# Kernel tuning notes

Measured on AMD Instinct MI355X. Metric: run time of the kernel, lower is better.

Reference implementation:

```python
import jax, jax.numpy as jnp
import numpy as np

L, D, H, DH, W, G, FF = 2, 768, 12, 64, 256, 64, 3072  # W = one-sided window (attention_window=512)
B, S = 2, 4096
NEG = -1e9


def setup_inputs() -> dict:
    key = jax.random.key(0)
    ks = jax.random.split(key, 16)
    inp = {}
    inp['hidden_states'] = jax.random.normal(ks[0], (B, S, D), jnp.float32)
    # HF Longformer convention: <0 masked, >0 global, 0 local. First G tokens are global.
    inp['attention_mask'] = jnp.zeros((B, S), jnp.float32).at[:, :G].set(1.0)
    inp['padding_len'] = 0
    inp['level_hierarchy'] = 0
    def w(k, shape):
        return (jax.random.normal(k, shape, jnp.float32) * 0.02)
    for i, n in enumerate(['Wq', 'Wk', 'Wv', 'Wqg', 'Wkg', 'Wvg', 'Wo']):
        inp[n] = w(ks[1 + i], (L, D, D))
        inp['b' + n[1:].lower()] = jnp.zeros((L, D), jnp.float32)
    inp['Wi'] = w(ks[8], (L, D, FF)); inp['bi'] = jnp.zeros((L, FF), jnp.float32)
    inp['Wo2'] = w(ks[9], (L, FF, D)); inp['bo2'] = jnp.zeros((L, D), jnp.float32)
    for n in ['ln1', 'ln2']:
        inp[n + '_g'] = jnp.ones((L, D), jnp.float32)
        inp[n + '_b'] = jnp.zeros((L, D), jnp.float32)
    return inp


def _ln(x, g, b):
    mu = jnp.mean(x, -1, keepdims=True)
    var = jnp.mean(jnp.square(x - mu), -1, keepdims=True)
    return (x - mu) * jax.lax.rsqrt(var + 1e-5) * g + b


def _chunk3(x, nc, w):
    # x: [..., S, d] -> [..., nc, 3w, d]: keys of chunks (c-1, c, c+1), zero-padded at the ends
    shp = x.shape
    xr = x.reshape(shp[:-2] + (nc, w, shp[-1]))
    pad = [(0, 0)] * xr.ndim
    pad[-3] = (1, 1)
    xp = jnp.pad(xr, pad)
    return jnp.concatenate([xp[..., :-2, :, :], xp[..., 1:-1, :, :], xp[..., 2:, :, :]], axis=-2)


def _layer(h, mask, Wq, bq, Wk, bk, Wv, bv, Wqg, bqg, Wkg, bkg, Wvg, bvg,
           Wo, bo, ln1_g, ln1_b, Wi, bi, Wo2, bo2, ln2_g, ln2_b):
    Bb, Ss, Dd = h.shape
    nc = Ss // W
    scale = 1.0 / np.sqrt(DH)
    def heads(x):
        return x.reshape(Bb, Ss, H, DH).transpose(0, 2, 1, 3)  # [B,H,S,dh]
    q = heads(h @ Wq + bq) * scale
    k = heads(h @ Wk + bk)
    v = heads(h @ Wv + bv)
    # --- sliding-window (banded) attention, chunked ---
    qc = q.reshape(Bb, H, nc, W, DH)
    k3 = _chunk3(k, nc, W)  # [B,H,nc,3W,dh]
    v3 = _chunk3(v, nc, W)
    local = jnp.einsum('bhcid,bhcjd->bhcij', qc, k3)  # [B,H,nc,W,3W]
    i = jnp.arange(W)[:, None]
    j = jnp.arange(3 * W)[None, :]
    band_ok = jnp.abs(j - W - i) <= W                              # [W,3W]
    keypos = jnp.arange(nc)[:, None, None] * W + (j - W)[None]     # [nc,1,3W]
    in_range = (keypos >= 0) & (keypos < Ss)
    # masked and global keys are removed from the windowed attention (handled via global cols)
    key_local = _chunk3((mask == 0).astype(h.dtype)[..., None], nc, W)[..., 0] > 0.5  # [B,nc,3W]
    valid = band_ok[None, None] & in_range[None] & key_local[:, :, None, :]  # [B,nc,W,3W]
    local = jnp.where(valid[:, None], local, NEG)
    # --- global key columns (every token attends to the G global tokens) ---
    kg, vg = k[:, :, :G], v[:, :, :G]
    sg = jnp.einsum('bhsd,bhgd->bhsg', q, kg).reshape(Bb, H, nc, W, G)
    probs = jax.nn.softmax(jnp.concatenate([sg, local], axis=-1), axis=-1)
    pg, pl = probs[..., :G], probs[..., G:]
    out = (jnp.einsum('bhcig,bhgd->bhcid', pg, vg)
           + jnp.einsum('bhcij,bhcjd->bhcid', pl, v3)).reshape(Bb, H, Ss, DH)
    # --- global token rows: full attention with dedicated global projections ---
    qg = heads(h @ Wqg + bqg)[:, :, :G] * scale
    kgf = heads(h @ Wkg + bkg)
    vgf = heads(h @ Wvg + bvg)
    add = jnp.where(mask < 0, NEG, 0.0)[:, None, None, :]
    pgl = jax.nn.softmax(jnp.einsum('bhgd,bhsd->bhgs', qg, kgf) + add, axis=-1)
    out = out.at[:, :, :G].set(jnp.einsum('bhgs,bhsd->bhgd', pgl, vgf))
    out = jnp.where((mask < 0)[:, None, :, None], 0.0, out)
    attn = out.transpose(0, 2, 1, 3).reshape(Bb, Ss, Dd) @ Wo + bo
    h = _ln(attn + h, ln1_g, ln1_b)
    ff = jax.nn.gelu(h @ Wi + bi, approximate=False) @ Wo2 + bo2
    return _ln(ff + h, ln2_g, ln2_b)


def reference(hidden_states, attention_mask, padding_len, level_hierarchy,
              Wq, bq, Wk, bk, Wv, bv, Wqg, bqg, Wkg, bkg, Wvg, bvg,
              Wo, bo, ln1_g, ln1_b, Wi, bi, Wo2, bo2, ln2_g, ln2_b):
    h = hidden_states
    for l in range(L):
        h = _layer(h, attention_mask,
                   Wq[l], bq[l], Wk[l], bk[l], Wv[l], bv[l],
                   Wqg[l], bqg[l], Wkg[l], bkg[l], Wvg[l], bvg[l],
                   Wo[l], bo[l], ln1_g[l], ln1_b[l],
                   Wi[l], bi[l], Wo2[l], bo2[l], ln2_g[l], ln2_b[l])
    if padding_len > 0:
        h = h[:, :-padding_len]
    return h
```

## Files before the change

### kernel.cpp

```cpp
#include <hip/hip_runtime.h>

#define B_ 2
#define S_ 4096
#define D_ 768
#define H_ 12
#define DH_ 64
#define W_ 256
#define G_ 64
#define FF_ 3072
#define L_ 2
#define M_ (B_*S_)
#define NEGV -1e9f
#define NSPLIT 16

typedef short bf16x8 __attribute__((ext_vector_type(8)));
typedef float f32x4 __attribute__((ext_vector_type(4)));
typedef unsigned short u16;
typedef unsigned short u16x4 __attribute__((ext_vector_type(4)));

__device__ __forceinline__ u16 f2bf(float f) {
  union { float f; unsigned u; } a; a.f = f;
  unsigned r = a.u + 0x7FFFu + ((a.u >> 16) & 1u);
  return (u16)(r >> 16);
}
__device__ __forceinline__ float b2f(u16 u) {
  union { unsigned u; float f; } a; a.u = ((unsigned)u) << 16;
  return a.f;
}

__device__ __forceinline__ f32x4 mfma16(bf16x8 a, bf16x8 b, f32x4 c) {
  return __builtin_amdgcn_mfma_f32_16x16x32_bf16(a, b, c, 0, 0, 0);
}

__device__ __forceinline__ void gload16(const u16* g, u16* l) {
  __builtin_amdgcn_global_load_lds((const __attribute__((address_space(1))) void*)g,
                                   (__attribute__((address_space(3))) void*)l, 16, 0, 0);
}

__device__ __forceinline__ int xcd_swz(int bid, int nwg) {
  if ((nwg & 7) == 0) {
    int cpx = nwg >> 3;
    bid = (bid & 7) * cpx + (bid >> 3);
  }
  return bid;
}

struct Ptr7 { const float* p[7]; };
__global__ __launch_bounds__(256) void wtrans7(Ptr7 in, u16* __restrict__ out) {
  __shared__ float tile[32][33];
  int z = blockIdx.z;
  int slab = z >> 1, l = z & 1;
  const float* src = in.p[slab] + (size_t)l * D_ * D_;
  u16* dst = out + (size_t)z * D_ * D_;
  int k0 = blockIdx.y * 32, n0 = blockIdx.x * 32;
  int tx = threadIdx.x, ty = threadIdx.y;
#pragma unroll
  for (int i = 0; i < 4; i++)
    tile[ty + i*8][tx] = src[(size_t)(k0 + ty + i*8) * D_ + n0 + tx];
  __syncthreads();
#pragma unroll
  for (int i = 0; i < 4; i++)
    dst[(size_t)(n0 + ty + i*8) * D_ + k0 + tx] = f2bf(tile[tx][ty + i*8]);
}

__global__ __launch_bounds__(256) void wtrans(const float* __restrict__ in,
                                              u16* __restrict__ out, int K, int N) {
  __shared__ float tile[32][33];
  size_t base = (size_t)blockIdx.z * K * N;
  int k0 = blockIdx.y * 32, n0 = blockIdx.x * 32;
  int tx = threadIdx.x, ty = threadIdx.y;
#pragma unroll
  for (int i = 0; i < 4; i++)
    tile[ty + i*8][tx] = in[base + (size_t)(k0 + ty + i*8) * N + n0 + tx];
  __syncthreads();
#pragma unroll
  for (int i = 0; i < 4; i++)
    out[base + (size_t)(n0 + ty + i*8) * K + k0 + tx] = f2bf(tile[tx][ty + i*8]);
}

__global__ __launch_bounds__(256) void conv_b(const float* __restrict__ in,
                                              u16* __restrict__ outb, int n4) {
  int i = blockIdx.x * 256 + threadIdx.x;
  if (i >= n4) return;
  float4 v = ((const float4*)in)[i];
  u16x4 o;
  o[0] = f2bf(v.x); o[1] = f2bf(v.y); o[2] = f2bf(v.z); o[3] = f2bf(v.w);
  ((u16x4*)outb)[i] = o;
}

template <int MODE>
__device__ __forceinline__ float epi_post(float v) {
  if (MODE == 2) return v * 0.125f;
  if (MODE == 3) {
    float y = 0.79788456f * (v + 0.044715f * v * v * v);
    float e = __expf(fminf(2.f * y, 20.f));
    return v * e / (e + 1.f);
  }
  return v;
}

struct Bias6 { const float* p[6]; };

template <int MODE, int NW>
__global__ __launch_bounds__(512, 4) void gemm_wide(const u16* __restrict__ A,
                                                    const u16* __restrict__ Wbase,
                                                    Bias6 bp,
                                                    u16* __restrict__ OutBase,
                                                    int Kdim, int Nstride, int l) {
  __shared__ u16 sh[36864];
  int gx = gridDim.x;
  int bid = blockIdx.x + blockIdx.y * gx;
  bid = xcd_swz(bid, gx * gridDim.y);
  int bxx = bid % gx, by = bid / gx;
  int bm = by * 128;
  int widx, bn;
  const u16* Bt; u16* Cb; const float* bias;
  bool qscale = false;
  if (NW == 5) {
    widx = bxx / 3;
    bn = (bxx % 3) * 256;
    int slab;
    if (widx == 5) {
      if (by != 0 && by != 32) return;
      slab = 3; qscale = true;
    } else {
      slab = widx + (widx >= 3 ? 1 : 0);
      qscale = (widx == 0);
    }
    Bt = Wbase + ((size_t)slab * L_ + l) * (size_t)D_ * D_;
    Cb = OutBase + (size_t)slab * M_ * D_;
    bias = bp.p[widx];
  } else {
    widx = 0;
    bn = bxx * 256;
    Bt = Wbase; Cb = OutBase; bias = bp.p[0];
  }
  int tid = threadIdx.x;
  int lane = tid & 63, wid = tid >> 6;
  int wr = wid >> 2, wc = wid & 3;
  int lr = lane & 15, lg = lane >> 4;

  int fA = tid;
  int lA_ = fA >> 3, uA = (fA & 7) ^ (lA_ & 7);
  int rowA = lA_ * 2 + (uA >> 2), c8A = uA & 3;
  const u16* srcA = A + (size_t)(bm + rowA) * Kdim + c8A * 8;
  int fB0 = tid, fB1 = tid + 512;
  int lB0 = fB0 >> 3, uB0 = (fB0 & 7) ^ (lB0 & 7);
  int rB0 = lB0 * 2 + (uB0 >> 2), c8B0 = uB0 & 3;
  int lB1 = fB1 >> 3, uB1 = (fB1 & 7) ^ (lB1 & 7);
  int rB1 = lB1 * 2 + (uB1 >> 2), c8B1 = uB1 & 3;
  const u16* srcB0 = Bt + (size_t)(bn + rB0) * Kdim + c8B0 * 8;
  const u16* srcB1 = Bt + (size_t)(bn + rB1) * Kdim + c8B1 * 8;

  auto stage = [&](int kt, int buf) {
    int k1 = kt << 5;
    gload16(srcA + k1, &sh[buf * 4096 + fA * 8]);
    gload16(srcB0 + k1, &sh[12288 + buf * 8192 + fB0 * 8]);
    gload16(srcB1 + k1, &sh[12288 + buf * 8192 + fB1 * 8]);
  };

  int offa[4], offb[4];
#pragma unroll
  for (int i = 0; i < 4; i++) {
    int ra = wr * 64 + i * 16 + lr;
    int la = ra >> 1, sa = (((ra & 1) << 2) | lg) ^ (la & 7);
    offa[i] = la * 64 + sa * 8;
    int rb = wc * 64 + i * 16 + lr;
    int lb = rb >> 1, sb = (((rb & 1) << 2) | lg) ^ (lb & 7);
    offb[i] = lb * 64 + sb * 8;
  }

  int nt = Kdim >> 5;
  f32x4 acc[4][4] = {};

  stage(0, 0);
  if (nt > 1) stage(1, 1);

  for (int t = 0; t < nt; t++) {
    int cb = t % 3;
    if (t + 2 < nt) {
      stage(t + 2, (t + 2) % 3);
      asm volatile("s_waitcnt vmcnt(6)" ::: "memory");
    } else if (t + 1 < nt) {
      asm volatile("s_waitcnt vmcnt(3)" ::: "memory");
    } else {
      asm volatile("s_waitcnt vmcnt(0)" ::: "memory");
    }
    __builtin_amdgcn_s_barrier();
    __builtin_amdgcn_sched_barrier(0);
    const u16* ab = sh + cb * 4096;
    const u16* bb = sh + 12288 + cb * 8192;
    bf16x8 a[4], b[4];
#pragma unroll
    for (int i = 0; i < 4; i++) a[i] = *(const bf16x8*)&ab[offa[i]];
#pragma unroll
    for (int j = 0; j < 4; j++) b[j] = *(const bf16x8*)&bb[offb[j]];
    __builtin_amdgcn_s_setprio(1);
#pragma unroll
    for (int i = 0; i < 4; i++)
#pragma unroll
      for (int j = 0; j < 4; j++)
        acc[i][j] = mfma16(a[i], b[j], acc[i][j]);
    __builtin_amdgcn_s_setprio(0);
    __builtin_amdgcn_sched_barrier(0);
    __builtin_amdgcn_s_barrier();
    __builtin_amdgcn_sched_barrier(0);
  }

  int r0 = bm + wr * 64, c0 = bn + wc * 64;
  int cr = (lane >> 4) * 4, cc = lane & 15;
  float sc = qscale ? 0.125f : 1.0f;
#pragma unroll
  for (int j = 0; j < 4; j++) {
    int col = c0 + j * 16 + cc;
    float bv = bias[col];
#pragma unroll
    for (int i = 0; i < 4; i++)
#pragma unroll
      for (int r = 0; r < 4; r++) {
        size_t off = (size_t)(r0 + i * 16 + cr + r) * Nstride + col;
        Cb[off] = f2bf(epi_post<MODE>((acc[i][j][r] + bv) * sc));
      }
  }
}

template <int MODE>
__global__ __launch_bounds__(256) void gemm_pipe(const u16* __restrict__ A,
                                                 const u16* __restrict__ Bt,
                                                 const float* __restrict__ bias,
                                                 u16* __restrict__ Cb,
                                                 int Ndim, int Kdim, int rowTileStride) {
  __shared__ u16 sh[24576];
  int gx = gridDim.x;
  int bid = blockIdx.x + blockIdx.y * gx;
  bid = xcd_swz(bid, gx * gridDim.y);
  int bm = (bid / gx) * rowTileStride * 128;
  int bn = (bid % gx) * 128;
  int tid = threadIdx.x;
  int lane = tid & 63, w = tid >> 6;
  int r0w = (w >> 1) * 64, c0w = (w & 1) * 64;
  int lr = lane & 15, lg = lane >> 4;

  int f0 = tid, l0 = f0 >> 3, s0 = (f0 & 7) ^ (l0 & 7);
  int row0 = (l0 << 1) | (s0 >> 2), c0s = (s0 & 3) * 8;
  int f1 = tid + 256, l1 = f1 >> 3, s1 = (f1 & 7) ^ (l1 & 7);
  int row1 = (l1 << 1) | (s1 >> 2), c1s = (s1 & 3) * 8;
  const u16* A0 = A + (size_t)(bm + row0) * Kdim + c0s;
  const u16* A1 = A + (size_t)(bm + row1) * Kdim + c1s;
  const u16* B0 = Bt + (size_t)(bn + row0) * Kdim + c0s;
  const u16* B1 = Bt + (size_t)(bn + row1) * Kdim + c1s;

  int offa[4], offb[4];
#pragma unroll
  for (int i = 0; i < 4; i++) {
    int ra = r0w + i * 16 + lr;
    int la = ra >> 1, sa = ((ra & 1) << 2) | lg;
    offa[i] = la * 64 + (sa ^ (la & 7)) * 8;
    int rb = c0w + i * 16 + lr;
    int lb = rb >> 1, sb = ((rb & 1) << 2) | lg;
    offb[i] = lb * 64 + (sb ^ (lb & 7)) * 8;
  }

  auto stage = [&](int kt, int buf) {
    int k1 = kt << 5;
    u16* ab = sh + buf * 4096;
    u16* bb = sh + 12288 + buf * 4096;
    gload16(A0 + k1, &ab[tid * 8]);
    gload16(A1 + k1, &ab[tid * 8 + 2048]);
    gload16(B0 + k1, &bb[tid * 8]);
    gload16(B1 + k1, &bb[tid * 8 + 2048]);
  };

  int nt = Kdim >> 5;
  f32x4 acc[4][4] = {};

  stage(0, 0);
  if (nt > 1) stage(1, 1);

  for (int t = 0; t < nt; t++) {
    int cb = t % 3;
    if (t + 2 < nt) {
      stage(t + 2, (t + 2) % 3);
      asm volatile("s_waitcnt vmcnt(8)" ::: "memory");
    } else if (t + 1 < nt) {
      asm volatile("s_waitcnt vmcnt(4)" ::: "memory");
    } else {
      asm volatile("s_waitcnt vmcnt(0)" ::: "memory");
    }
    __builtin_amdgcn_s_barrier();
    __builtin_amdgcn_sched_barrier(0);
    const u16* ab = sh + cb * 4096;
    const u16* bb = sh + 12288 + cb * 4096;
    bf16x8 a[4], b[4];
#pragma unroll
    for (int i = 0; i < 4; i++) a[i] = *(const bf16x8*)&ab[offa[i]];
#pragma unroll
    for (int j = 0; j < 4; j++) b[j] = *(const bf16x8*)&bb[offb[j]];
#pragma unroll
    for (int i = 0; i < 4; i++)
#pragma unroll
      for (int j = 0; j < 4; j++)
        acc[i][j] = mfma16(a[i], b[j], acc[i][j]);
    __builtin_amdgcn_sched_barrier(0);
    __builtin_amdgcn_s_barrier();
    __builtin_amdgcn_sched_barrier(0);
  }

  int cr = (lane >> 4) * 4, cc = lane & 15;
#pragma unroll
  for (int j = 0; j < 4; j++) {
    int col = c0w + j * 16 + cc;
    float bv = bias[bn + col];
#pragma unroll
    for (int i = 0; i < 4; i++)
#pragma unroll
      for (int r = 0; r < 4; r++) {
        int row = r0w + i * 16 + cr + r;
        int chunk = (col >> 3) ^ (row & 15);
        sh[row * 128 + chunk * 8 + (col & 7)] =
            f2bf(epi_post<MODE>(acc[i][j][r] + bv));
      }
  }
  __syncthreads();
  {
    int row = tid >> 1, half = tid & 1;
    u16* gro = Cb + (size_t)(bm + row) * Ndim + bn + half * 64;
#pragma unroll
    for (int c = 0; c < 8; c++) {
      int lc = half * 8 + c;
      int pc = lc ^ (row & 15);
      bf16x8 v = *(const bf16x8*)&sh[row * 128 + pc * 8];
      *(bf16x8*)(gro + c * 8) = v;
    }
  }
}

__global__ __launch_bounds__(128) void attn_local(const u16* __restrict__ qb,
                                                  const u16* __restrict__ kb_,
                                                  const u16* __restrict__ vb,
                                                  const float* __restrict__ mask,
                                                  u16* __restrict__ ao) {
  int bid = blockIdx.x + blockIdx.y * gridDim.x;
  bid = xcd_swz(bid, 1536);
  int cx = bid & 63, bh = bid >> 6;
  int c = cx >> 2, sub = cx & 3;
  int b = bh / H_, h = bh % H_;
  int tid = threadIdx.x;
  int w = tid >> 6, lane = tid & 63;
  int lr = lane & 15, lg = lane >> 4;

  __shared__ u16 vtT[64][72];
  __shared__ u16 plds[2][32][72];
  __shared__ unsigned char vflag[576];

  int base_off = sub * 64;
  int kwin0 = c * W_ - W_;
  for (int i = tid; i < 576; i += 128) {
    int kp = kwin0 + base_off + i;
    vflag[i] = (kp >= 0 && kp < S_ && mask[b * S_ + kp] == 0.0f) ? 1 : 0;
  }

  size_t hoff = (size_t)b * S_ * D_ + h * DH_;
  int qrow0 = c * W_ + base_off + w * 32;
  bf16x8 aq[2][2];
#pragma unroll
  for (int fi = 0; fi < 2; fi++)
#pragma unroll
    for (int ks = 0; ks < 2; ks++)
      aq[fi][ks] = *(const bf16x8*)(qb + hoff + (size_t)(qrow0 + fi * 16 + lr) * D_ + ks * 32 + lg * 8);

  int K0 = kwin0 + base_off;
  int kb_lo = (K0 < 0) ? (1 + ((-K0) >> 6)) : 1;
  int kb_hi = 9;
  { int hi = 1 + ((S_ - 64 - K0) >> 6); if (hi < 9) kb_hi = hi; }
  int niter = 1 + (kb_hi - kb_lo + 1);

  int stg_k4 = tid >> 3, stg_j = tid & 7;
  int stg_dh0 = stg_j * 8;

  float ls[2][4];
  f32x4 o[2][4] = {};
#pragma unroll
  for (int fi = 0; fi < 2; fi++)
#pragma unroll
    for (int r = 0; r < 4; r++) ls[fi][r] = 0.f;

  bf16x8 ck0[4], ck1[4], nk0[4], nk1[4], cv[4], nv[4];
#pragma unroll
  for (int nj = 0; nj < 4; nj++) {
    const u16* ks8 = kb_ + hoff + (size_t)(nj * 16 + lr) * D_ + lg * 8;
    ck0[nj] = *(const bf16x8*)(ks8);
    ck1[nj] = *(const bf16x8*)(ks8 + 32);
  }
#pragma unroll
  for (int p = 0; p < 4; p++)
    cv[p] = *(const bf16x8*)(vb + hoff + (size_t)(p * 16 + stg_k4) * D_ + stg_dh0);

  for (int it = 0; it < niter; it++) {
    int kb = (it == 0) ? 0 : (kb_lo + it - 1);

    __builtin_amdgcn_s_barrier();
#pragma unroll
    for (int p = 0; p < 4; p++) {
      int key = p * 16 + stg_k4;
      u16* basep = &vtT[stg_dh0][key ^ (stg_j << 3)];
#pragma unroll
      for (int e = 0; e < 8; e++) basep[e * 72] = (u16)cv[p][e];
    }
    if (it + 1 < niter) {
      int kb2 = kb_lo + it;
      int ks2 = K0 + (kb2 - 1) * 64;
#pragma unroll
      for (int nj = 0; nj < 4; nj++) {
        const u16* ks8 = kb_ + hoff + (size_t)(ks2 + nj * 16 + lr) * D_ + lg * 8;
        nk0[nj] = *(const bf16x8*)(ks8);
        nk1[nj] = *(const bf16x8*)(ks8 + 32);
      }
#pragma unroll
      for (int p = 0; p < 4; p++)
        nv[p] = *(const bf16x8*)(vb + hoff + (size_t)(ks2 + p * 16 + stg_k4) * D_ + stg_dh0);
    }
    asm volatile("s_waitcnt lgkmcnt(0)" ::: "memory");
    __builtin_amdgcn_s_barrier();
    __builtin_amdgcn_sched_barrier(0);

    f32x4 sc[2][4];
#pragma unroll
    for (int fi = 0; fi < 2; fi++)
#pragma unroll
      for (int nj = 0; nj < 4; nj++) {
        f32x4 t = {};
        t = mfma16(aq[fi][0], ck0[nj], t);
        t = mfma16(aq[fi][1], ck1[nj], t);
        sc[fi][nj] = t;
      }

    if (kb >= 2 && kb <= 8) {
#pragma unroll
      for (int nj = 0; nj < 4; nj++) {
        bool kv = vflag[(kb - 1) * 64 + nj * 16 + lr] != 0;
#pragma unroll
        for (int fi = 0; fi < 2; fi++)
#pragma unroll
          for (int r = 0; r < 4; r++)
            sc[fi][nj][r] = kv ? sc[fi][nj][r] : NEGV;
      }
    } else if (kb > 0) {
#pragma unroll
      for (int nj = 0; nj < 4; nj++) {
        int fidx = (kb - 1) * 64 + nj * 16 + lr;
        int koff = base_off + fidx;
        bool kv = vflag[fidx] != 0;
#pragma unroll
        for (int fi = 0; fi < 2; fi++)
#pragma unroll
          for (int r = 0; r < 4; r++) {
            int wq = base_off + w * 32 + fi * 16 + lg * 4 + r;
            if (!(kv && koff >= wq && koff <= wq + 2 * W_)) sc[fi][nj][r] = NEGV;
          }
      }
    }

#pragma unroll
    for (int fi = 0; fi < 2; fi++)
#pragma unroll
      for (int r = 0; r < 4; r++) {
        float ps = 0.f;
#pragma unroll
        for (int nj = 0; nj < 4; nj++) {
          float p = __expf(sc[fi][nj][r]);
          sc[fi][nj][r] = p;
          ps += p;
        }
#pragma unroll
        for (int d = 1; d < 16; d <<= 1) ps += __shfl_xor(ps, d);
        ls[fi][r] += ps;
      }

#pragma unroll
    for (int fi = 0; fi < 2; fi++)
#pragma unroll
      for (int nj = 0; nj < 4; nj++)
#pragma unroll
        for (int r = 0; r < 4; r++)
          plds[w][fi * 16 + lg * 4 + r][nj * 16 + lr] = f2bf(sc[fi][nj][r]);
    asm volatile("s_waitcnt lgkmcnt(0)" ::: "memory");
    __builtin_amdgcn_sched_barrier(0);

    bf16x8 ap[2][2];
#pragma unroll
    for (int fi = 0; fi < 2; fi++)
#pragma unroll
      for (int ks = 0; ks < 2; ks++)
        ap[fi][ks] = *(const bf16x8*)&plds[w][fi * 16 + lr][ks * 32 + lg * 8];
#pragma unroll
    for (int dj = 0; dj < 4; dj++) {
      int xr = ((dj * 16 + lr) >> 3) & 7;
#pragma unroll
      for (int ks = 0; ks < 2; ks++) {
        bf16x8 bv = *(const bf16x8*)&vtT[dj * 16 + lr][(ks * 32 + lg * 8) ^ (xr << 3)];
        o[0][dj] = mfma16(ap[0][ks], bv, o[0][dj]);
        o[1][dj] = mfma16(ap[1][ks], bv, o[1][dj]);
      }
    }

    if (it + 1 < niter) {
#pragma unroll
      for (int j = 0; j < 4; j++) {
        ck0[j] = nk0[j]; ck1[j] = nk1[j]; cv[j] = nv[j];
      }
    }
  }

#pragma unroll
  for (int fi = 0; fi < 2; fi++)
#pragma unroll
    for (int dj = 0; dj < 4; dj++)
#pragma unroll
      for (int r = 0; r < 4; r++) {
        int row = qrow0 + fi * 16 + lg * 4 + r;
        float v = o[fi][dj][r] / ls[fi][r];
        ao[hoff + (size_t)row * D_ + dj * 16 + lr] = f2bf(v);
      }
}

__global__ __launch_bounds__(128) void attn_gsplit(const u16* __restrict__ qg,
                                                   const u16* __restrict__ kg,
                                                   const u16* __restrict__ vg,
                                                   float* __restrict__ opart,
                                                   float* __restrict__ lpart) {
  int sp = blockIdx.x, bh = blockIdx.y;
  int b = bh / H_, h = bh % H_;
  int tid = threadIdx.x, w = tid >> 6, lane = tid & 63;
  int lr = lane & 15, lg = lane >> 4;
  __shared__ u16 vtT[64][72];
  __shared__ u16 plds[2][32][72];
  size_t hoff = (size_t)b * S_ * D_ + h * DH_;
  int qrow0 = w * 32;
  bf16x8 aq[2][2];
#pragma unroll
  for (int fi = 0; fi < 2; fi++)
#pragma unroll
    for (int ks = 0; ks < 2; ks++)
      aq[fi][ks] = *(const bf16x8*)(qg + hoff + (size_t)(qrow0 + fi * 16 + lr) * D_ + ks * 32 + lg * 8);
  float ls[2][4];
  f32x4 o[2][4] = {};
#pragma unroll
  for (int fi = 0; fi < 2; fi++)
#pragma unroll
    for (int r = 0; r < 4; r++) ls[fi][r] = 0.f;

  int stg_k4 = tid >> 3, stg_j = tid & 7;
  int stg_dh0 = stg_j * 8;

  for (int kb = 0; kb < 4; kb++) {
    int kstart = sp * 256 + kb * 64;
    __syncthreads();
#pragma unroll
    for (int p = 0; p < 4; p++) {
      int key = p * 16 + stg_k4;
      bf16x8 row = *(const bf16x8*)(vg + hoff + (size_t)(kstart + key) * D_ + stg_dh0);
      u16* basep = &vtT[stg_dh0][key ^ (stg_j << 3)];
#pragma unroll
      for (int e = 0; e < 8; e++) basep[e * 72] = (u16)row[e];
    }
    __syncthreads();

    bf16x8 bk0[4], bk1[4];
#pragma unroll
    for (int nj = 0; nj < 4; nj++) {
      const u16* ks8 = kg + hoff + (size_t)(kstart + nj * 16 + lr) * D_ + lg * 8;
      bk0[nj] = *(const bf16x8*)(ks8);
      bk1[nj] = *(const bf16x8*)(ks8 + 32);
    }
    f32x4 sc[2][4];
#pragma unroll
    for (int fi = 0; fi < 2; fi++)
#pragma unroll
      for (int nj = 0; nj < 4; nj++) {
        f32x4 t = {};
        t = mfma16(aq[fi][0], bk0[nj], t);
        t = mfma16(aq[fi][1], bk1[nj], t);
        sc[fi][nj] = t;
      }
#pragma unroll
    for (int fi = 0; fi < 2; fi++)
#pragma unroll
      for (int r = 0; r < 4; r++) {
        float ps = 0.f;
#pragma unroll
        for (int nj = 0; nj < 4; nj++) {
          float p = __expf(sc[fi][nj][r]);
          sc[fi][nj][r] = p;
          ps += p;
        }
#pragma unroll
        for (int d = 1; d < 16; d <<= 1) ps += __shfl_xor(ps, d);
        ls[fi][r] += ps;
      }
#pragma unroll
    for (int fi = 0; fi < 2; fi++)
#pragma unroll
      for (int nj = 0; nj < 4; nj++)
#pragma unroll
        for (int r = 0; r < 4; r++)
          plds[w][fi * 16 + lg * 4 + r][nj * 16 + lr] = f2bf(sc[fi][nj][r]);
    asm volatile("s_waitcnt lgkmcnt(0)" ::: "memory");
    __builtin_amdgcn_sched_barrier(0);
    bf16x8 ap[2][2];
#pragma unroll
    for (int fi = 0; fi < 2; fi++)
#pragma unroll
      for (int ks = 0; ks < 2; ks++)
        ap[fi][ks] = *(const bf16x8*)&plds[w][fi * 16 + lr][ks * 32 + lg * 8];
#pragma unroll
    for (int dj = 0; dj < 4; dj++) {
      int xr = ((dj * 16 + lr) >> 3) & 7;
#pragma unroll
      for (int ks = 0; ks < 2; ks++) {
        bf16x8 bv = *(const bf16x8*)&vtT[dj * 16 + lr][(ks * 32 + lg * 8) ^ (xr << 3)];
        o[0][dj] = mfma16(ap[0][ks], bv, o[0][dj]);
        o[1][dj] = mfma16(ap[1][ks], bv, o[1][dj]);
      }
    }
  }

  size_t pbase = (size_t)(bh * NSPLIT + sp) * 64;
#pragma unroll
  for (int fi = 0; fi < 2; fi++)
#pragma unroll
    for (int r = 0; r < 4; r++) {
      int row = qrow0 + fi * 16 + lg * 4 + r;
      if (lr == 0) lpart[pbase + row] = ls[fi][r];
#pragma unroll
      for (int dj = 0; dj < 4; dj++)
        opart[(pbase + row) * 64 + dj * 16 + lr] = o[fi][dj][r];
    }
}

__global__ __launch_bounds__(256) void attn_gcombine(const float* __restrict__ opart,
                                                     const float* __restrict__ lpart,
                                                     u16* __restrict__ ao) {
  int bh = blockIdx.x;
  int b = bh / H_, h = bh % H_;
  int t = threadIdx.x;
  __shared__ float lt[64];
  if (t < 64) {
    float lsum = 0.f;
#pragma unroll
    for (int sp = 0; sp < NSPLIT; sp++)
      lsum += lpart[(size_t)(bh * NSPLIT + sp) * 64 + t];
    lt[t] = lsum;
  }
  __syncthreads();
  int row = t >> 2, c0 = (t & 3) * 16;
  float acc[16] = {};
  for (int sp = 0; sp < NSPLIT; sp++) {
    const float* op = opart + ((size_t)(bh * NSPLIT + sp) * 64 + row) * 64 + c0;
#pragma unroll
    for (int j = 0; j < 16; j++) acc[j] += op[j];
  }
  float inv = 1.f / lt[row];
  size_t hoff = (size_t)b * S_ * D_ + h * DH_;
#pragma unroll
  for (int j = 0; j < 16; j++)
    ao[hoff + (size_t)row * D_ + c0 + j] = f2bf(acc[j] * inv);
}

__global__ __launch_bounds__(192) void ln_b(const u16* __restrict__ x,
                                            const u16* __restrict__ res,
                                            const float* __restrict__ gg,
                                            const float* __restrict__ bb,
                                            u16* __restrict__ outb,
                                            float* __restrict__ outf) {
  int row = blockIdx.x, t = threadIdx.x;
  const u16* xr = x + (size_t)row * D_;
  const u16* rr = res + (size_t)row * D_;
  u16x4 xv = *(const u16x4*)&xr[t * 4];
  u16x4 rv = *(const u16x4*)&rr[t * 4];
  float v[4];
#pragma unroll
  for (int e = 0; e < 4; e++) v[e] = b2f(xv[e]) + b2f(rv[e]);
  __shared__ float sha[3], shb[3];
  float s = v[0] + v[1] + v[2] + v[3];
#pragma unroll
  for (int d = 1; d < 64; d <<= 1) s += __shfl_xor(s, d);
  if ((t & 63) == 0) sha[t >> 6] = s;
  __syncthreads();
  float mu = (sha[0] + sha[1] + sha[2]) * (1.f / 768.f);
  float dd[4], s2 = 0.f;
#pragma unroll
  for (int e = 0; e < 4; e++) { dd[e] = v[e] - mu; s2 += dd[e] * dd[e]; }
#pragma unroll
  for (int d = 1; d < 64; d <<= 1) s2 += __shfl_xor(s2, d);
  if ((t & 63) == 0) shb[t >> 6] = s2;
  __syncthreads();
  float var = (shb[0] + shb[1] + shb[2]) * (1.f / 768.f);
  float rs = rsqrtf(var + 1e-5f);
  float4 gv = *(const float4*)&gg[t * 4];
  float4 bv = *(const float4*)&bb[t * 4];
  float y0 = dd[0] * rs * gv.x + bv.x;
  float y1 = dd[1] * rs * gv.y + bv.y;
  float y2 = dd[2] * rs * gv.z + bv.z;
  float y3 = dd[3] * rs * gv.w + bv.w;
  u16x4 ov;
  ov[0] = f2bf(y0); ov[1] = f2bf(y1); ov[2] = f2bf(y2); ov[3] = f2bf(y3);
  *(u16x4*)&outb[(size_t)row * D_ + t * 4] = ov;
  if (outf) {
    float4 of = {y0, y1, y2, y3};
    *(float4*)&outf[(size_t)row * D_ + t * 4] = of;
  }
}

extern "C" void kernel_launch(void* const* d_in, const int* in_sizes, int n_in,
                              void* d_out, int out_size, void* d_ws, size_t ws_size,
                              hipStream_t stream) {
  (void)in_sizes; (void)n_in; (void)out_size; (void)ws_size;
  const float* hidden = (const float*)d_in[0];
  const float* mask   = (const float*)d_in[1];
  const float* Wq  = (const float*)d_in[4];   const float* bq  = (const float*)d_in[5];
  const float* Wk  = (const float*)d_in[6];   const float* bk  = (const float*)d_in[7];
  const float* Wv  = (const float*)d_in[8];   const float* bv  = (const float*)d_in[9];
  const float* Wqg = (const float*)d_in[10];  const float* bqg = (const float*)d_in[11];
  const float* Wkg = (const float*)d_in[12];  const float* bkg = (const float*)d_in[13];
  const float* Wvg = (const float*)d_in[14];  const float* bvg = (const float*)d_in[15];
  const float* Wo  = (const float*)d_in[16];  const float* bo  = (const float*)d_in[17];
  const float* Wi  = (const float*)d_in[18];  const float* bi  = (const float*)d_in[19];
  const float* Wo2 = (const float*)d_in[20];  const float* bo2 = (const float*)d_in[21];
  const float* ln1g = (const float*)d_in[22]; const float* ln1b = (const float*)d_in[23];
  const float* ln2g = (const float*)d_in[24]; const float* ln2b = (const float*)d_in[25];

  char* ws = (char*)d_ws;
  size_t off = 0;
  auto alloc = [&](size_t bytes) -> void* {
    void* p = ws + off;
    off += (bytes + 255) & ~(size_t)255;
    return p;
  };
  const size_t DD = (size_t)D_ * D_;
  const size_t DF = (size_t)D_ * FF_;
  u16* Wt = (u16*)alloc((7 * L_ * DD + 2 * L_ * DF) * 2);
  u16* wo_t  = Wt + 6 * L_ * DD;
  u16* wi_t  = Wt + 7 * L_ * DD;
  u16* wo2_t = Wt + 7 * L_ * DD + L_ * DF;

  u16* X0 = (u16*)alloc((size_t)M_ * D_ * 2);
  u16* X1 = (u16*)alloc((size_t)M_ * D_ * 2);
  u16* tb = (u16*)alloc((size_t)M_ * D_ * 2);
  u16* B_bf = (u16*)alloc((size_t)M_ * FF_ * 2);
  u16* qbf  = (u16*)alloc((size_t)M_ * D_ * 2 * 6);
  u16* kbf  = qbf + 1 * (size_t)M_ * D_;
  u16* vbf  = qbf + 2 * (size_t)M_ * D_;
  u16* qgbf = qbf + 3 * (size_t)M_ * D_;
  u16* kgbf = qbf + 4 * (size_t)M_ * D_;
  u16* vgbf = qbf + 5 * (size_t)M_ * D_;
  u16* aobf = (u16*)alloc((size_t)M_ * D_ * 2);
  float* opart = (float*)alloc((size_t)B_ * H_ * NSPLIT * 64 * 64 * 4);
  float* lpart = (float*)alloc((size_t)B_ * H_ * NSPLIT * 64 * 4);

  dim3 tb32(32, 8);
  Ptr7 wp;
  wp.p[0] = Wq; wp.p[1] = Wk; wp.p[2] = Wv; wp.p[3] = Wqg;
  wp.p[4] = Wkg; wp.p[5] = Wvg; wp.p[6] = Wo;
  wtrans7<<<dim3(24, 24, 14), tb32, 0, stream>>>(wp, Wt);
  wtrans<<<dim3(96, 24, 2), tb32, 0, stream>>>(Wi,  wi_t,  D_, FF_);
  wtrans<<<dim3(24, 96, 2), tb32, 0, stream>>>(Wo2, wo2_t, FF_, D_);

  conv_b<<<(M_ * D_ / 4 + 255) / 256, 256, 0, stream>>>(hidden, X0, M_ * D_ / 4);

  for (int l = 0; l < L_; l++) {
    size_t wdd = (size_t)l * DD;
    size_t wdf = (size_t)l * DF;
    dim3 g64(6, 64);

    Bias6 bp;
    bp.p[0] = bq  + l * D_;
    bp.p[1] = bk  + l * D_;
    bp.p[2] = bv  + l * D_;
    bp.p[3] = bkg + l * D_;
    bp.p[4] = bvg + l * D_;
    bp.p[5] = bqg + l * D_;
    gemm_wide<1, 5><<<dim3(18, 64), 512, 0, stream>>>(X0, Wt, bp, qbf, D_, D_, l);

    attn_local<<<dim3((S_ / W_) * 4, B_ * H_), 128, 0, stream>>>(qbf, kbf, vbf, mask, aobf);
    attn_gsplit<<<dim3(NSPLIT, B_ * H_), 128, 0, stream>>>(qgbf, kgbf, vgbf, opart, lpart);
    attn_gcombine<<<B_ * H_, 256, 0, stream>>>(opart, lpart, aobf);

    gemm_pipe<1><<<g64, 256, 0, stream>>>(aobf, wo_t + wdd, bo + l * D_, tb, D_, D_, 1);
    ln_b<<<M_, 192, 0, stream>>>(tb, X0, ln1g + l * D_, ln1b + l * D_, X1, nullptr);

    Bias6 bpi; bpi.p[0] = bi + l * FF_;
    gemm_wide<3, 1><<<dim3(12, 64), 512, 0, stream>>>(X1, wi_t + wdf, bpi, B_bf, D_, FF_, 0);
    gemm_pipe<1><<<g64, 256, 0, stream>>>(B_bf, wo2_t + wdf, bo2 + l * D_, tb, D_, FF_, 1);

    ln_b<<<M_, 192, 0, stream>>>(tb, X1, ln2g + l * D_, ln2b + l * D_, X0,
                                 (l == L_ - 1) ? (float*)d_out : nullptr);
  }
}
```

Measured before the change: 650.1 us.

## Write V projections transposed from GEMM epilogue and load V fragments directly

The QKV GEMM epilogue now writes the V and global-V outputs in a transposed [B, D, S] layout into a new buffer. Both attention kernels then load V MFMA operands straight from global memory instead of staging V through a transposed shared-memory tile with barriers. This removes the shared-memory transpose and its two per-iteration barriers. In exchange the GEMM epilogue does strided 8-byte stores, and attention reads V from global memory without register prefetch, which exposes load latency inside each iteration.

```diff
diff --git a/kernel.cpp b/kernel.cpp
--- a/kernel.cpp
+++ b/kernel.cpp
@@ -106,6 +106,7 @@
                                                     const u16* __restrict__ Wbase,
                                                     Bias6 bp,
                                                     u16* __restrict__ OutBase,
+                                                    u16* __restrict__ VtB,
                                                     int Kdim, int Nstride, int l) {
   __shared__ u16 sh[36864];
   int gx = gridDim.x;
@@ -209,6 +210,26 @@
 
   int r0 = bm + wr * 64, c0 = bn + wc * 64;
   int cr = (lane >> 4) * 4, cc = lane & 15;
+
+  if (NW == 5 && (widx == 2 || widx == 4)) {
+    u16* Vt = VtB + (widx == 4 ? (size_t)M_ * D_ : 0);
+#pragma unroll
+    for (int j = 0; j < 4; j++) {
+      int col = c0 + j * 16 + cc;
+      float bv = bias[col];
+#pragma unroll
+      for (int i = 0; i < 4; i++) {
+        int srow = r0 + i * 16 + cr;
+        int bb2 = srow >> 12, ss = srow & 4095;
+        u16x4 ov;
+#pragma unroll
+        for (int r = 0; r < 4; r++) ov[r] = f2bf(acc[i][j][r] + bv);
+        *(u16x4*)&Vt[((size_t)(bb2 * D_ + col) << 12) + ss] = ov;
+      }
+    }
+    return;
+  }
+
   float sc = qscale ? 0.125f : 1.0f;
 #pragma unroll
   for (int j = 0; j < 4; j++) {
@@ -337,7 +358,7 @@
 
 __global__ __launch_bounds__(128) void attn_local(const u16* __restrict__ qb,
                                                   const u16* __restrict__ kb_,
-                                                  const u16* __restrict__ vb,
+                                                  const u16* __restrict__ vt,
                                                   const float* __restrict__ mask,
                                                   u16* __restrict__ ao) {
   int bid = blockIdx.x + blockIdx.y * gridDim.x;
@@ -349,7 +370,6 @@
   int w = tid >> 6, lane = tid & 63;
   int lr = lane & 15, lg = lane >> 4;
 
-  __shared__ u16 vtT[64][72];
   __shared__ u16 plds[2][32][72];
   __shared__ unsigned char vflag[576];
 
@@ -359,8 +379,10 @@
     int kp = kwin0 + base_off + i;
     vflag[i] = (kp >= 0 && kp < S_ && mask[b * S_ + kp] == 0.0f) ? 1 : 0;
   }
+  __syncthreads();
 
   size_t hoff = (size_t)b * S_ * D_ + h * DH_;
+  const u16* vth = vt + ((size_t)(b * D_ + h * DH_) << 12);
   int qrow0 = c * W_ + base_off + w * 32;
   bf16x8 aq[2][2];
 #pragma unroll
@@ -375,9 +397,6 @@
   { int hi = 1 + ((S_ - 64 - K0) >> 6); if (hi < 9) kb_hi = hi; }
   int niter = 1 + (kb_hi - kb_lo + 1);
 
-  int stg_k4 = tid >> 3, stg_j = tid & 7;
-  int stg_dh0 = stg_j * 8;
-
   float ls[2][4];
   f32x4 o[2][4] = {};
 #pragma unroll
@@ -385,44 +404,17 @@
 #pragma unroll
     for (int r = 0; r < 4; r++) ls[fi][r] = 0.f;
 
-  bf16x8 ck0[4], ck1[4], nk0[4], nk1[4], cv[4], nv[4];
+  bf16x8 ck0[4], ck1[4], nk0[4], nk1[4];
 #pragma unroll
   for (int nj = 0; nj < 4; nj++) {
     const u16* ks8 = kb_ + hoff + (size_t)(nj * 16 + lr) * D_ + lg * 8;
     ck0[nj] = *(const bf16x8*)(ks8);
     ck1[nj] = *(const bf16x8*)(ks8 + 32);
   }
-#pragma unroll
-  for (int p = 0; p < 4; p++)
-    cv[p] = *(const bf16x8*)(vb + hoff + (size_t)(p * 16 + stg_k4) * D_ + stg_dh0);
 
   for (int it = 0; it < niter; it++) {
     int kb = (it == 0) ? 0 : (kb_lo + it - 1);
-
-    __builtin_amdgcn_s_barrier();
-#pragma unroll
-    for (int p = 0; p < 4; p++) {
-      int key = p * 16 + stg_k4;
-      u16* basep = &vtT[stg_dh0][key ^ (stg_j << 3)];
-#pragma unroll
-      for (int e = 0; e < 8; e++) basep[e * 72] = (u16)cv[p][e];
-    }
-    if (it + 1 < niter) {
-      int kb2 = kb_lo + it;
-      int ks2 = K0 + (kb2 - 1) * 64;
-#pragma unroll
-      for (int nj = 0; nj < 4; nj++) {
-        const u16* ks8 = kb_ + hoff + (size_t)(ks2 + nj * 16 + lr) * D_ + lg * 8;
-        nk0[nj] = *(const bf16x8*)(ks8);
-        nk1[nj] = *(const bf16x8*)(ks8 + 32);
-      }
-#pragma unroll
-      for (int p = 0; p < 4; p++)
-        nv[p] = *(const bf16x8*)(vb + hoff + (size_t)(ks2 + p * 16 + stg_k4) * D_ + stg_dh0);
-    }
-    asm volatile("s_waitcnt lgkmcnt(0)" ::: "memory");
-    __builtin_amdgcn_s_barrier();
-    __builtin_amdgcn_sched_barrier(0);
+    int kstart = (it == 0) ? 0 : (K0 + (kb - 1) * 64);
 
     f32x4 sc[2][4];
 #pragma unroll
@@ -435,6 +427,23 @@
         sc[fi][nj] = t;
       }
 
+    bf16x8 vf[4][2];
+#pragma unroll
+    for (int dj = 0; dj < 4; dj++)
+#pragma unroll
+      for (int ks = 0; ks < 2; ks++)
+        vf[dj][ks] = *(const bf16x8*)&vth[((size_t)(dj * 16 + lr) << 12) + kstart + ks * 32 + lg * 8];
+
+    if (it + 1 < niter) {
+      int ks2 = K0 + (kb_lo + it - 1) * 64;
+#pragma unroll
+      for (int nj = 0; nj < 4; nj++) {
+        const u16* ks8 = kb_ + hoff + (size_t)(ks2 + nj * 16 + lr) * D_ + lg * 8;
+        nk0[nj] = *(const bf16x8*)(ks8);
+        nk1[nj] = *(const bf16x8*)(ks8 + 32);
+      }
+    }
+
     if (kb >= 2 && kb <= 8) {
 #pragma unroll
       for (int nj = 0; nj < 4; nj++) {
@@ -494,20 +503,17 @@
       for (int ks = 0; ks < 2; ks++)
         ap[fi][ks] = *(const bf16x8*)&plds[w][fi * 16 + lr][ks * 32 + lg * 8];
 #pragma unroll
-    for (int dj = 0; dj < 4; dj++) {
-      int xr = ((dj * 16 + lr) >> 3) & 7;
+    for (int dj = 0; dj < 4; dj++)
 #pragma unroll
       for (int ks = 0; ks < 2; ks++) {
-        bf16x8 bv = *(const bf16x8*)&vtT[dj * 16 + lr][(ks * 32 + lg * 8) ^ (xr << 3)];
-        o[0][dj] = mfma16(ap[0][ks], bv, o[0][dj]);
-        o[1][dj] = mfma16(ap[1][ks], bv, o[1][dj]);
-      }
-    }
+        o[0][dj] = mfma16(ap[0][ks], vf[dj][ks], o[0][dj]);
+        o[1][dj] = mfma16(ap[1][ks], vf[dj][ks], o[1][dj]);
+      }
 
     if (it + 1 < niter) {
 #pragma unroll
       for (int j = 0; j < 4; j++) {
-        ck0[j] = nk0[j]; ck1[j] = nk1[j]; cv[j] = nv[j];
+        ck0[j] = nk0[j]; ck1[j] = nk1[j];
       }
     }
   }
@@ -526,16 +532,16 @@
 
 __global__ __launch_bounds__(128) void attn_gsplit(const u16* __restrict__ qg,
                                                    const u16* __restrict__ kg,
-                                                   const u16* __restrict__ vg,
+                                                   const u16* __restrict__ vgt,
                                                    float* __restrict__ opart,
                                                    float* __restrict__ lpart) {
   int sp = blockIdx.x, bh = blockIdx.y;
   int b = bh / H_, h = bh % H_;
   int tid = threadIdx.x, w = tid >> 6, lane = tid & 63;
   int lr = lane & 15, lg = lane >> 4;
-  __shared__ u16 vtT[64][72];
   __shared__ u16 plds[2][32][72];
   size_t hoff = (size_t)b * S_ * D_ + h * DH_;
+  const u16* vth = vgt + ((size_t)(b * D_ + h * DH_) << 12);
   int qrow0 = w * 32;
   bf16x8 aq[2][2];
 #pragma unroll
@@ -550,21 +556,8 @@
 #pragma unroll
     for (int r = 0; r < 4; r++) ls[fi][r] = 0.f;
 
-  int stg_k4 = tid >> 3, stg_j = tid & 7;
-  int stg_dh0 = stg_j * 8;
-
   for (int kb = 0; kb < 4; kb++) {
     int kstart = sp * 256 + kb * 64;
-    __syncthreads();
-#pragma unroll
-    for (int p = 0; p < 4; p++) {
-      int key = p * 16 + stg_k4;
-      bf16x8 row = *(const bf16x8*)(vg + hoff + (size_t)(kstart + key) * D_ + stg_dh0);
-      u16* basep = &vtT[stg_dh0][key ^ (stg_j << 3)];
-#pragma unroll
-      for (int e = 0; e < 8; e++) basep[e * 72] = (u16)row[e];
-    }
-    __syncthreads();
 
     bf16x8 bk0[4], bk1[4];
 #pragma unroll
@@ -573,6 +566,13 @@
       bk0[nj] = *(const bf16x8*)(ks8);
       bk1[nj] = *(const bf16x8*)(ks8 + 32);
     }
+    bf16x8 vf[4][2];
+#pragma unroll
+    for (int dj = 0; dj < 4; dj++)
+#pragma unroll
+      for (int ks = 0; ks < 2; ks++)
+        vf[dj][ks] = *(const bf16x8*)&vth[((size_t)(dj * 16 + lr) << 12) + kstart + ks * 32 + lg * 8];
+
     f32x4 sc[2][4];
 #pragma unroll
     for (int fi = 0; fi < 2; fi++)
@@ -614,15 +614,12 @@
       for (int ks = 0; ks < 2; ks++)
         ap[fi][ks] = *(const bf16x8*)&plds[w][fi * 16 + lr][ks * 32 + lg * 8];
 #pragma unroll
-    for (int dj = 0; dj < 4; dj++) {
-      int xr = ((dj * 16 + lr) >> 3) & 7;
+    for (int dj = 0; dj < 4; dj++)
 #pragma unroll
       for (int ks = 0; ks < 2; ks++) {
-        bf16x8 bv = *(const bf16x8*)&vtT[dj * 16 + lr][(ks * 32 + lg * 8) ^ (xr << 3)];
-        o[0][dj] = mfma16(ap[0][ks], bv, o[0][dj]);
-        o[1][dj] = mfma16(ap[1][ks], bv, o[1][dj]);
-      }
-    }
+        o[0][dj] = mfma16(ap[0][ks], vf[dj][ks], o[0][dj]);
+        o[1][dj] = mfma16(ap[1][ks], vf[dj][ks], o[1][dj]);
+      }
   }
 
   size_t pbase = (size_t)(bh * NSPLIT + sp) * 64;
@@ -750,10 +747,10 @@
   u16* B_bf = (u16*)alloc((size_t)M_ * FF_ * 2);
   u16* qbf  = (u16*)alloc((size_t)M_ * D_ * 2 * 6);
   u16* kbf  = qbf + 1 * (size_t)M_ * D_;
-  u16* vbf  = qbf + 2 * (size_t)M_ * D_;
   u16* qgbf = qbf + 3 * (size_t)M_ * D_;
   u16* kgbf = qbf + 4 * (size_t)M_ * D_;
-  u16* vgbf = qbf + 5 * (size_t)M_ * D_;
+  u16* vtb  = (u16*)alloc((size_t)M_ * D_ * 2 * 2);
+  u16* vgt  = vtb + (size_t)M_ * D_;
   u16* aobf = (u16*)alloc((size_t)M_ * D_ * 2);
   float* opart = (float*)alloc((size_t)B_ * H_ * NSPLIT * 64 * 64 * 4);
   float* lpart = (float*)alloc((size_t)B_ * H_ * NSPLIT * 64 * 4);
@@ -780,17 +777,17 @@
     bp.p[3] = bkg + l * D_;
     bp.p[4] = bvg + l * D_;
     bp.p[5] = bqg + l * D_;
-    gemm_wide<1, 5><<<dim3(18, 64), 512, 0, stream>>>(X0, Wt, bp, qbf, D_, D_, l);
-
-    attn_local<<<dim3((S_ / W_) * 4, B_ * H_), 128, 0, stream>>>(qbf, kbf, vbf, mask, aobf);
-    attn_gsplit<<<dim3(NSPLIT, B_ * H_), 128, 0, stream>>>(qgbf, kgbf, vgbf, opart, lpart);
+    gemm_wide<1, 5><<<dim3(18, 64), 512, 0, stream>>>(X0, Wt, bp, qbf, vtb, D_, D_, l);
+
+    attn_local<<<dim3((S_ / W_) * 4, B_ * H_), 128, 0, stream>>>(qbf, kbf, vtb, mask, aobf);
+    attn_gsplit<<<dim3(NSPLIT, B_ * H_), 128, 0, stream>>>(qgbf, kgbf, vgt, opart, lpart);
     attn_gcombine<<<B_ * H_, 256, 0, stream>>>(opart, lpart, aobf);
 
     gemm_pipe<1><<<g64, 256, 0, stream>>>(aobf, wo_t + wdd, bo + l * D_, tb, D_, D_, 1);
     ln_b<<<M_, 192, 0, stream>>>(tb, X0, ln1g + l * D_, ln1b + l * D_, X1, nullptr);
 
     Bias6 bpi; bpi.p[0] = bi + l * FF_;
-    gemm_wide<3, 1><<<dim3(12, 64), 512, 0, stream>>>(X1, wi_t + wdf, bpi, B_bf, D_, FF_, 0);
+    gemm_wide<3, 1><<<dim3(12, 64), 512, 0, stream>>>(X1, wi_t + wdf, bpi, B_bf, nullptr, D_, FF_, 0);
     gemm_pipe<1><<<g64, 256, 0, stream>>>(B_bf, wo2_t + wdf, bo2 + l * D_, tb, D_, FF_, 1);
 
     ln_b<<<M_, 192, 0, stream>>>(tb, X1, ln2g + l * D_, ln2b + l * D_, X0,
```

Measured after the change: 647.0 us. No clear change (-0.5%).
